# Kernel optimization log

Hardware: AMD Instinct MI355X
Metric: run time of the kernel (lower is better)

## Reference

```python
import jax, jax.numpy as jnp
import numpy as np

EMBED = 1024
HEADS = 16
HEAD_DIM = EMBED // HEADS


def setup_inputs() -> dict:
    key = jax.random.key(0)
    ks = jax.random.split(key, 6)
    s = 1.0 / np.sqrt(EMBED)
    return {
        "x": jax.random.normal(ks[0], (2, 2048, EMBED), dtype=jnp.float32),
        "Wq": jax.random.normal(ks[1], (EMBED, EMBED), dtype=jnp.float32) * s,
        "Wk": jax.random.normal(ks[2], (EMBED, EMBED), dtype=jnp.float32) * s,
        "Wv": jax.random.normal(ks[3], (EMBED, EMBED), dtype=jnp.float32) * s,
        "Wfc": jax.random.normal(ks[4], (EMBED, EMBED), dtype=jnp.float32) * s,
        "bfc": jnp.zeros((EMBED,), dtype=jnp.float32),
    }


def reference(x, Wq, Wk, Wv, Wfc, bfc):
    # x: (N, L, E). Linear(E,E,bias=False) applies y = x @ W.T (torch convention).
    N, L, E = x.shape
    q = (x @ Wq.T).reshape(N, L, HEADS, HEAD_DIM)
    k = (x @ Wk.T).reshape(N, L, HEADS, HEAD_DIM)
    v = (x @ Wv.T).reshape(N, L, HEADS, HEAD_DIM)
    # energy: (N, H, Q, K)
    energy = jnp.einsum('nqhd,nkhd->nhqk', q, k)
    # NOTE: original scales by sqrt(embed_size), not sqrt(head_dim)
    attn = jax.nn.softmax(energy / jnp.sqrt(jnp.float32(E)), axis=3)
    out = jnp.einsum('nhql,nlhd->nqhd', attn, v).reshape(N, L, E)
    return out @ Wfc.T + bfc
```

## Files before the change

kernel.cpp:

```cpp
#include <hip/hip_runtime.h>
#include <stdint.h>


typedef short bf16x8 __attribute__((ext_vector_type(8)));
typedef short bf16x4 __attribute__((ext_vector_type(4)));
typedef float f32x4 __attribute__((ext_vector_type(4)));

__device__ __forceinline__ unsigned short f2bf(float f) {
  union { float f; unsigned u; } v; v.f = f;
  return (unsigned short)((v.u + 0x7FFFu + ((v.u >> 16) & 1u)) >> 16);
}

#if defined(__has_builtin)
#if __has_builtin(__builtin_amdgcn_cvt_pk_bf16_f32)
#define HAVE_PK_BF16 1
#endif
#if __has_builtin(__builtin_amdgcn_exp2f)
#define EXP2(x) __builtin_amdgcn_exp2f(x)
#endif
#endif
#ifndef EXP2
#define EXP2(x) exp2f(x)
#endif

__device__ __forceinline__ unsigned pk2bf(float a, float b) {
#ifdef HAVE_PK_BF16
  typedef __bf16 bfv2 __attribute__((ext_vector_type(2)));
  union { bfv2 v; unsigned u; } c;
  c.v = __builtin_amdgcn_cvt_pk_bf16_f32(a, b);
  return c.u;
#else
  return (unsigned)f2bf(a) | ((unsigned)f2bf(b) << 16);
#endif
}

__device__ __forceinline__ void load_lds16(const unsigned short* g, unsigned short* l) {
  __builtin_amdgcn_global_load_lds(
      (const __attribute__((address_space(1))) unsigned int*)(const void*)g,
      (__attribute__((address_space(3))) unsigned int*)(void*)l, 16, 0, 0);
}

#define MFMA16(a, b, c) __builtin_amdgcn_mfma_f32_16x16x32_bf16((a), (b), (c), 0, 0, 0)

#if defined(__has_builtin)
#if __has_builtin(__builtin_amdgcn_mfma_f32_16x16x16bf16_1k)
#define MFMAK16(a, b, c) __builtin_amdgcn_mfma_f32_16x16x16bf16_1k((a), (b), (c), 0, 0, 0)
#elif __has_builtin(__builtin_amdgcn_mfma_f32_16x16x16_bf16)
#define MFMAK16(a, b, c) __builtin_amdgcn_mfma_f32_16x16x16_bf16((a), (b), (c), 0, 0, 0)
#endif
#endif
#ifndef MFMAK16
__device__ __forceinline__ f32x4 mfmak16_asm(bf16x4 a, bf16x4 b, f32x4 c) {
  asm volatile("v_mfma_f32_16x16x16_bf16 %0, %1, %2, %0" : "+v"(c) : "v"(a), "v"(b));
  return c;
}
#define MFMAK16(a, b, c) mfmak16_asm((a), (b), (c))
#endif

__global__ __launch_bounds__(256) void cvt_all_kernel(
    const float* __restrict__ x, const float* __restrict__ w0, const float* __restrict__ w1,
    const float* __restrict__ w2, const float* __restrict__ w3, unsigned short* __restrict__ xb,
    unsigned short* __restrict__ d0, unsigned short* __restrict__ d1,
    unsigned short* __restrict__ d2, unsigned short* __restrict__ d3) {
  int i = blockIdx.x * 256 + threadIdx.x;
  const float* s;
  unsigned short* d;
  int off;
  if (i < 1048576) {
    s = x; d = xb; off = i;
  } else {
    int j = i - 1048576;
    int w = j >> 18;
    off = j & 262143;
    s = (w == 0) ? w0 : (w == 1) ? w1 : (w == 2) ? w2 : w3;
    d = (w == 0) ? d0 : (w == 1) ? d1 : (w == 2) ? d2 : d3;
  }
  float4 f = ((const float4*)s)[off];
  uint2 o;
  o.x = pk2bf(f.x, f.y);
  o.y = pk2bf(f.z, f.w);
  ((uint2*)d)[off] = o;
}

__global__ __launch_bounds__(256) void gemm_qkv_kernel(
    const unsigned short* __restrict__ Xb, const unsigned short* __restrict__ Wqb,
    const unsigned short* __restrict__ Wkb, const unsigned short* __restrict__ Wvb,
    unsigned short* __restrict__ Qo, unsigned short* __restrict__ Ko,
    unsigned short* __restrict__ Vt) {
  __shared__ __align__(16) unsigned short As[128 * 32];
  __shared__ __align__(16) unsigned short Bs[128 * 32];
  const int mode = blockIdx.z;
  const unsigned short* W = (mode == 0) ? Wqb : ((mode == 1) ? Wkb : Wvb);
  const int n0 = blockIdx.x * 128;
  const int m0 = blockIdx.y * 128;
  const int tid = threadIdx.x;
  const int lane = tid & 63;
  const int wv = tid >> 6;
  const int wm = (wv >> 1) * 64;
  const int wn = (wv & 1) * 64;
  const int qq = lane >> 4;
  const int cc = lane & 15;

  const f32x4 fz = {0.f, 0.f, 0.f, 0.f};
  f32x4 acc[4][4];
#pragma unroll
  for (int i = 0; i < 4; i++)
#pragma unroll
    for (int j = 0; j < 4; j++) acc[i][j] = fz;

  const int ia0 = tid, ia1 = tid + 256;
  const int ra0 = ia0 >> 2, ca0 = (ia0 & 3) * 8;
  const int ra1 = ia1 >> 2, ca1 = (ia1 & 3) * 8;

  for (int k0 = 0; k0 < 1024; k0 += 32) {
    __syncthreads();
    load_lds16(Xb + (m0 + ra0) * 1024 + k0 + ca0, As + ia0 * 8);
    load_lds16(Xb + (m0 + ra1) * 1024 + k0 + ca1, As + ia1 * 8);
    load_lds16(W + (n0 + ra0) * 1024 + k0 + ca0, Bs + ia0 * 8);
    load_lds16(W + (n0 + ra1) * 1024 + k0 + ca1, Bs + ia1 * 8);
    __syncthreads();
    bf16x8 a[4], b[4];
#pragma unroll
    for (int i = 0; i < 4; i++) a[i] = *(const bf16x8*)(As + (wm + i * 16 + cc) * 32 + qq * 8);
#pragma unroll
    for (int j = 0; j < 4; j++) b[j] = *(const bf16x8*)(Bs + (wn + j * 16 + cc) * 32 + qq * 8);
    if (mode < 2) {
#pragma unroll
      for (int i = 0; i < 4; i++)
#pragma unroll
        for (int j = 0; j < 4; j++) acc[i][j] = MFMA16(b[j], a[i], acc[i][j]);
    } else {
#pragma unroll
      for (int i = 0; i < 4; i++)
#pragma unroll
        for (int j = 0; j < 4; j++) acc[i][j] = MFMA16(a[i], b[j], acc[i][j]);
    }
  }

  if (mode < 2) {
    const float esc = (mode == 0) ? 0.0450842200277801f : 1.0f;
    unsigned short* dst = (mode == 0) ? Qo : Ko;
#pragma unroll
    for (int i = 0; i < 4; i++) {
      int row = m0 + wm + i * 16 + cc;
#pragma unroll
      for (int j = 0; j < 4; j++) {
        int col = n0 + wn + j * 16 + qq * 4;
        uint2 pk;
        pk.x = pk2bf(acc[i][j][0] * esc, acc[i][j][1] * esc);
        pk.y = pk2bf(acc[i][j][2] * esc, acc[i][j][3] * esc);
        *(uint2*)(dst + row * 1024 + col) = pk;
      }
    }
  } else {
#pragma unroll
    for (int i = 0; i < 4; i++)
#pragma unroll
      for (int j = 0; j < 4; j++) {
        int row = m0 + wm + i * 16 + qq * 4;
        int nn = row >> 11, ll = row & 2047;
        int col = n0 + wn + j * 16 + cc;
        int hh = col >> 6, dd = col & 63;
        uint2 pk;
        pk.x = pk2bf(acc[i][j][0], acc[i][j][1]);
        pk.y = pk2bf(acc[i][j][2], acc[i][j][3]);
        *(uint2*)(Vt + ((nn * 16 + hh) * 64 + dd) * 2048 + ll) = pk;
      }
  }
}

__global__ __launch_bounds__(256, 2) void attn_kernel(const unsigned short* __restrict__ Qg,
                                                      const unsigned short* __restrict__ Kg,
                                                      const unsigned short* __restrict__ Vg,
                                                      unsigned short* __restrict__ Og) {
  __shared__ __align__(16) unsigned short smem[2][128 * 64 + 64 * 128];
  const int qt = blockIdx.x, hh = blockIdx.y, nb = blockIdx.z;
  const int tid = threadIdx.x, lane = tid & 63, wv = tid >> 6;
  const int pair = wv >> 1, wq = wv & 1;
  const int ptid = tid & 127;
  const int qq = lane >> 4, cc = lane & 15;
  const int q0 = qt * 128 + wq * 64;
  const int kb = pair * 1024;
  unsigned short* Kp = smem[pair];
  unsigned short* Vp = smem[pair] + 128 * 64;
  const unsigned short* Kbase = Kg + (size_t)(nb * 2048 + kb) * 1024 + hh * 64;
  const unsigned short* Vbase = Vg + (size_t)((nb * 16 + hh) * 64) * 2048 + kb;

  const int cK = ptid & 7, rKb = ptid >> 3;
  const int swK = (cK ^ (rKb & 7)) << 3;
  const int cV = ptid & 15, rVb = ptid >> 4;

  bf16x8 qf[4][2];
#pragma unroll
  for (int rt = 0; rt < 4; rt++)
#pragma unroll
    for (int kc = 0; kc < 2; kc++)
      qf[rt][kc] = *(const bf16x8*)(Qg + (size_t)(nb * 2048 + q0 + rt * 16 + cc) * 1024 +
                                    hh * 64 + kc * 32 + qq * 8);

  const f32x4 fz = {0.f, 0.f, 0.f, 0.f};
  const bf16x4 onesA = {(short)0x3F80, (short)0x3F80, (short)0x3F80, (short)0x3F80};
  f32x4 o[4][4];
  f32x4 lacc[4];
#pragma unroll
  for (int rt = 0; rt < 4; rt++) {
    lacc[rt] = fz;
#pragma unroll
    for (int vt = 0; vt < 4; vt++) o[rt][vt] = fz;
  }

  bf16x8 kbuf[8], vbuf[8];
#pragma unroll
  for (int p = 0; p < 8; p++)
    kbuf[p] = *(const bf16x8*)(Kbase + (size_t)(p * 16 + rKb) * 1024 + cK * 8);
#pragma unroll
  for (int p = 0; p < 8; p++)
    vbuf[p] = *(const bf16x8*)(Vbase + (size_t)(p * 8 + rVb) * 2048 + cV * 8);

#pragma unroll 1
  for (int it = 0; it < 8; it++) {
    __syncthreads();
#pragma unroll
    for (int p = 0; p < 8; p++) *(bf16x8*)(Kp + (p * 16 + rKb) * 64 + swK) = kbuf[p];
#pragma unroll
    for (int p = 0; p < 8; p++)
      *(bf16x8*)(Vp + (p * 8 + rVb) * 128 + ((cV ^ (((p & 1) << 3) | rVb)) << 3)) = vbuf[p];
    __syncthreads();
    if (it < 7) {
      const size_t ktn = (size_t)(it + 1) * 128;
#pragma unroll
      for (int p = 0; p < 8; p++)
        kbuf[p] = *(const bf16x8*)(Kbase + (ktn + p * 16 + rKb) * 1024 + cK * 8);
#pragma unroll
      for (int p = 0; p < 8; p++)
        vbuf[p] = *(const bf16x8*)(Vbase + (size_t)(p * 8 + rVb) * 2048 + ktn + cV * 8);
    }
#pragma unroll
    for (int st = 0; st < 8; st++) {
      const unsigned short* kr = Kp + (st * 16 + cc) * 64;
      int ch0 = (qq ^ (cc & 7)) << 3;
      bf16x8 k0 = *(const bf16x8*)(kr + ch0);
      bf16x8 k1 = *(const bf16x8*)(kr + (ch0 ^ 32));
      f32x4 z[4];
#pragma unroll
      for (int rt = 0; rt < 4; rt++) {
        z[rt] = MFMA16(k0, qf[rt][0], fz);
        z[rt] = MFMA16(k1, qf[rt][1], z[rt]);
      }
      bf16x4 bp[4];
#pragma unroll
      for (int rt = 0; rt < 4; rt++) {
        float p0 = EXP2(z[rt][0]), p1 = EXP2(z[rt][1]);
        float p2 = EXP2(z[rt][2]), p3 = EXP2(z[rt][3]);
        union { uint2 u; bf16x4 v; } pk;
        pk.u.x = pk2bf(p0, p1);
        pk.u.y = pk2bf(p2, p3);
        bp[rt] = pk.v;
        lacc[rt] = MFMAK16(onesA, bp[rt], lacc[rt]);
      }
      int vc = st * 2 + (qq >> 1);
      int voff = (qq & 1) * 4;
#pragma unroll
      for (int vt = 0; vt < 4; vt++) {
        bf16x4 vf = *(const bf16x4*)(Vp + (vt * 16 + cc) * 128 + ((vc ^ cc) << 3) + voff);
#pragma unroll
        for (int rt = 0; rt < 4; rt++) o[rt][vt] = MFMAK16(vf, bp[rt], o[rt][vt]);
      }
    }
  }

  float* oex = (float*)&smem[0][0];
  float* lex = oex + 8192;
  __syncthreads();
  if (pair == 1) {
#pragma unroll
    for (int rt = 0; rt < 4; rt++) {
#pragma unroll
      for (int vt = 0; vt < 4; vt++) {
        int idx = (((wq * 4 + rt) * 4 + vt) * 4 + qq) * 16 + cc;
        *(f32x4*)(oex + idx * 4) = o[rt][vt];
      }
      if (qq == 0) lex[(wq * 4 + rt) * 16 + cc] = lacc[rt][0];
    }
  }
  __syncthreads();
  if (pair == 0) {
#pragma unroll
    for (int rt = 0; rt < 4; rt++) {
      float rinv = 1.0f / (lacc[rt][0] + lex[(wq * 4 + rt) * 16 + cc]);
#pragma unroll
      for (int vt = 0; vt < 4; vt++) {
        int idx = (((wq * 4 + rt) * 4 + vt) * 4 + qq) * 16 + cc;
        f32x4 op = *(const f32x4*)(oex + idx * 4);
        uint2 ov;
        ov.x = pk2bf((o[rt][vt][0] + op[0]) * rinv, (o[rt][vt][1] + op[1]) * rinv);
        ov.y = pk2bf((o[rt][vt][2] + op[2]) * rinv, (o[rt][vt][3] + op[3]) * rinv);
        *(uint2*)(Og + (size_t)(nb * 2048 + q0 + rt * 16 + cc) * 1024 + hh * 64 + vt * 16 +
                  qq * 4) = ov;
      }
    }
  }
}

__global__ __launch_bounds__(256) void gemm_fc_kernel(const unsigned short* __restrict__ Ab,
                                                      const unsigned short* __restrict__ Wb,
                                                      const float* __restrict__ bias,
                                                      float* __restrict__ Co) {
  __shared__ __align__(16) unsigned short As[64 * 32];
  __shared__ __align__(16) unsigned short Bs[128 * 32];
  const int n0 = blockIdx.x * 128;
  const int m0 = blockIdx.y * 64;
  const int tid = threadIdx.x;
  const int lane = tid & 63;
  const int wv = tid >> 6;
  const int wm = (wv & 1) * 32;
  const int wn = (wv >> 1) * 64;
  const int qq = lane >> 4;
  const int cc = lane & 15;

  const f32x4 fz = {0.f, 0.f, 0.f, 0.f};
  f32x4 acc[2][4];
#pragma unroll
  for (int i = 0; i < 2; i++)
#pragma unroll
    for (int j = 0; j < 4; j++) acc[i][j] = fz;

  const int raA = tid >> 2, caA = (tid & 3) * 8;
  const int ia0 = tid, ia1 = tid + 256;
  const int rb0 = ia0 >> 2, cb0 = (ia0 & 3) * 8;
  const int rb1 = ia1 >> 2, cb1 = (ia1 & 3) * 8;

  for (int k0 = 0; k0 < 1024; k0 += 32) {
    __syncthreads();
    load_lds16(Ab + (m0 + raA) * 1024 + k0 + caA, As + tid * 8);
    load_lds16(Wb + (n0 + rb0) * 1024 + k0 + cb0, Bs + ia0 * 8);
    load_lds16(Wb + (n0 + rb1) * 1024 + k0 + cb1, Bs + ia1 * 8);
    __syncthreads();
    bf16x8 a[2], b[4];
#pragma unroll
    for (int i = 0; i < 2; i++) a[i] = *(const bf16x8*)(As + (wm + i * 16 + cc) * 32 + qq * 8);
#pragma unroll
    for (int j = 0; j < 4; j++) b[j] = *(const bf16x8*)(Bs + (wn + j * 16 + cc) * 32 + qq * 8);
#pragma unroll
    for (int i = 0; i < 2; i++)
#pragma unroll
      for (int j = 0; j < 4; j++) acc[i][j] = MFMA16(b[j], a[i], acc[i][j]);
  }

#pragma unroll
  for (int i = 0; i < 2; i++) {
    int row = m0 + wm + i * 16 + cc;
#pragma unroll
    for (int j = 0; j < 4; j++) {
      int col = n0 + wn + j * 16 + qq * 4;
      float4 bb = *(const float4*)(bias + col);
      float4 ov;
      ov.x = acc[i][j][0] + bb.x;
      ov.y = acc[i][j][1] + bb.y;
      ov.z = acc[i][j][2] + bb.z;
      ov.w = acc[i][j][3] + bb.w;
      *(float4*)(Co + (size_t)row * 1024 + col) = ov;
    }
  }
}

extern "C" void kernel_launch(void* const* d_in, const int* in_sizes, int n_in, void* d_out,
                              int out_size, void* d_ws, size_t ws_size, hipStream_t stream) {
  const float* x = (const float*)d_in[0];
  const float* Wq = (const float*)d_in[1];
  const float* Wk = (const float*)d_in[2];
  const float* Wv = (const float*)d_in[3];
  const float* Wfc = (const float*)d_in[4];
  const float* bfc = (const float*)d_in[5];
  float* out = (float*)d_out;
  char* ws = (char*)d_ws;
  unsigned short* xb = (unsigned short*)(ws);
  unsigned short* wqb = (unsigned short*)(ws + (8u << 20));
  unsigned short* wkb = (unsigned short*)(ws + (10u << 20));
  unsigned short* wvb = (unsigned short*)(ws + (12u << 20));
  unsigned short* wfb = (unsigned short*)(ws + (14u << 20));
  unsigned short* Qb = (unsigned short*)(ws + (16u << 20));
  unsigned short* Kb = (unsigned short*)(ws + (24u << 20));
  unsigned short* Vtb = (unsigned short*)(ws + (32u << 20));
  unsigned short* Ob = (unsigned short*)(ws + (40u << 20));

  cvt_all_kernel<<<8192, 256, 0, stream>>>(x, Wq, Wk, Wv, Wfc, xb, wqb, wkb, wvb, wfb);
  gemm_qkv_kernel<<<dim3(8, 32, 3), 256, 0, stream>>>(xb, wqb, wkb, wvb, Qb, Kb, Vtb);
  attn_kernel<<<dim3(16, 16, 2), 256, 0, stream>>>(Qb, Kb, Vtb, Ob);
  gemm_fc_kernel<<<dim3(8, 64), 256, 0, stream>>>(Ob, wfb, bfc, out);
}
```

Before: 212.0 us.

## Double-buffer K/V tiles via direct global-to-LDS loads and sum softmax in registers

The attention kernel now streams K and V in 64-key tiles into double-buffered shared memory using direct global-to-LDS loads, instead of staging 128-key tiles through registers. Loading the next tile while the current one is computed is meant to remove the register staging and one of the two barriers per iteration. The row-sum for the softmax denominator moves from an extra MFMA against a ones vector to scalar adds plus cross-lane shuffles at the end. This relies on a load_lds16 helper defined elsewhere, and it changes the V layout and swizzle in shared memory along with the tile size.

Result: faster. 200.8 us (-5.3%).

```diff
diff --git a/kernel.cpp b/kernel.cpp
--- a/kernel.cpp
+++ b/kernel.cpp
@@ -173,22 +173,18 @@
                                                       const unsigned short* __restrict__ Kg,
                                                       const unsigned short* __restrict__ Vg,
                                                       unsigned short* __restrict__ Og) {
-  __shared__ __align__(16) unsigned short smem[2][128 * 64 + 64 * 128];
+  __shared__ __align__(16) unsigned short smem[2][2][8192];
   const int qt = blockIdx.x, hh = blockIdx.y, nb = blockIdx.z;
   const int tid = threadIdx.x, lane = tid & 63, wv = tid >> 6;
   const int pair = wv >> 1, wq = wv & 1;
-  const int ptid = tid & 127;
   const int qq = lane >> 4, cc = lane & 15;
   const int q0 = qt * 128 + wq * 64;
-  const int kb = pair * 1024;
-  unsigned short* Kp = smem[pair];
-  unsigned short* Vp = smem[pair] + 128 * 64;
-  const unsigned short* Kbase = Kg + (size_t)(nb * 2048 + kb) * 1024 + hh * 64;
-  const unsigned short* Vbase = Vg + (size_t)((nb * 16 + hh) * 64) * 2048 + kb;
-
-  const int cK = ptid & 7, rKb = ptid >> 3;
-  const int swK = (cK ^ (rKb & 7)) << 3;
-  const int cV = ptid & 15, rVb = ptid >> 4;
+  const unsigned short* Kbase = Kg + (size_t)(nb * 2048 + pair * 1024) * 1024 + hh * 64;
+  const unsigned short* Vbase = Vg + (size_t)((nb * 16 + hh) * 64) * 2048 + pair * 1024;
+
+  const int lr = lane >> 3;
+  const int lc8 = ((lane & 7) ^ lr) * 8;
+  const int ldl = lane * 8;
 
   bf16x8 qf[4][2];
 #pragma unroll
@@ -199,44 +195,43 @@
                                     hh * 64 + kc * 32 + qq * 8);
 
   const f32x4 fz = {0.f, 0.f, 0.f, 0.f};
-  const bf16x4 onesA = {(short)0x3F80, (short)0x3F80, (short)0x3F80, (short)0x3F80};
   f32x4 o[4][4];
-  f32x4 lacc[4];
-#pragma unroll
-  for (int rt = 0; rt < 4; rt++) {
-    lacc[rt] = fz;
+  float lsum[4] = {0.f, 0.f, 0.f, 0.f};
+#pragma unroll
+  for (int rt = 0; rt < 4; rt++)
 #pragma unroll
     for (int vt = 0; vt < 4; vt++) o[rt][vt] = fz;
-  }
-
-  bf16x8 kbuf[8], vbuf[8];
-#pragma unroll
-  for (int p = 0; p < 8; p++)
-    kbuf[p] = *(const bf16x8*)(Kbase + (size_t)(p * 16 + rKb) * 1024 + cK * 8);
-#pragma unroll
-  for (int p = 0; p < 8; p++)
-    vbuf[p] = *(const bf16x8*)(Vbase + (size_t)(p * 8 + rVb) * 2048 + cV * 8);
+
+  {
+    unsigned short* Kb = &smem[pair][0][0];
+    unsigned short* Vb = &smem[pair][0][4096];
+#pragma unroll
+    for (int i = 0; i < 4; i++) {
+      int CI = wq * 4 + i;
+      load_lds16(Kbase + (size_t)(CI * 8 + lr) * 1024 + lc8, Kb + CI * 512 + ldl);
+      load_lds16(Vbase + (size_t)(CI * 8 + lr) * 2048 + lc8, Vb + CI * 512 + ldl);
+    }
+  }
+  __syncthreads();
 
 #pragma unroll 1
-  for (int it = 0; it < 8; it++) {
-    __syncthreads();
-#pragma unroll
-    for (int p = 0; p < 8; p++) *(bf16x8*)(Kp + (p * 16 + rKb) * 64 + swK) = kbuf[p];
-#pragma unroll
-    for (int p = 0; p < 8; p++)
-      *(bf16x8*)(Vp + (p * 8 + rVb) * 128 + ((cV ^ (((p & 1) << 3) | rVb)) << 3)) = vbuf[p];
-    __syncthreads();
-    if (it < 7) {
-      const size_t ktn = (size_t)(it + 1) * 128;
-#pragma unroll
-      for (int p = 0; p < 8; p++)
-        kbuf[p] = *(const bf16x8*)(Kbase + (ktn + p * 16 + rKb) * 1024 + cK * 8);
-#pragma unroll
-      for (int p = 0; p < 8; p++)
-        vbuf[p] = *(const bf16x8*)(Vbase + (size_t)(p * 8 + rVb) * 2048 + ktn + cV * 8);
-    }
-#pragma unroll
-    for (int st = 0; st < 8; st++) {
+  for (int it = 0; it < 16; it++) {
+    const int buf = it & 1;
+    if (it < 15) {
+      const int ktn = (it + 1) * 64;
+      unsigned short* Kb = &smem[pair][buf ^ 1][0];
+      unsigned short* Vb = &smem[pair][buf ^ 1][4096];
+#pragma unroll
+      for (int i = 0; i < 4; i++) {
+        int CI = wq * 4 + i;
+        load_lds16(Kbase + (size_t)(ktn + CI * 8 + lr) * 1024 + lc8, Kb + CI * 512 + ldl);
+        load_lds16(Vbase + (size_t)(CI * 8 + lr) * 2048 + ktn + lc8, Vb + CI * 512 + ldl);
+      }
+    }
+    const unsigned short* Kp = &smem[pair][buf][0];
+    const unsigned short* Vp = &smem[pair][buf][4096];
+#pragma unroll
+    for (int st = 0; st < 4; st++) {
       const unsigned short* kr = Kp + (st * 16 + cc) * 64;
       int ch0 = (qq ^ (cc & 7)) << 3;
       bf16x8 k0 = *(const bf16x8*)(kr + ch0);
@@ -252,24 +247,33 @@
       for (int rt = 0; rt < 4; rt++) {
         float p0 = EXP2(z[rt][0]), p1 = EXP2(z[rt][1]);
         float p2 = EXP2(z[rt][2]), p3 = EXP2(z[rt][3]);
+        lsum[rt] += (p0 + p1) + (p2 + p3);
         union { uint2 u; bf16x4 v; } pk;
         pk.u.x = pk2bf(p0, p1);
         pk.u.y = pk2bf(p2, p3);
         bp[rt] = pk.v;
-        lacc[rt] = MFMAK16(onesA, bp[rt], lacc[rt]);
       }
       int vc = st * 2 + (qq >> 1);
       int voff = (qq & 1) * 4;
 #pragma unroll
       for (int vt = 0; vt < 4; vt++) {
-        bf16x4 vf = *(const bf16x4*)(Vp + (vt * 16 + cc) * 128 + ((vc ^ cc) << 3) + voff);
+        bf16x4 vf = *(const bf16x4*)(Vp + (vt * 16 + cc) * 64 + ((vc ^ (cc & 7)) << 3) + voff);
 #pragma unroll
         for (int rt = 0; rt < 4; rt++) o[rt][vt] = MFMAK16(vf, bp[rt], o[rt][vt]);
       }
     }
-  }
-
-  float* oex = (float*)&smem[0][0];
+    __syncthreads();
+  }
+
+#pragma unroll
+  for (int rt = 0; rt < 4; rt++) {
+    float l = lsum[rt];
+    l += __shfl_xor(l, 16);
+    l += __shfl_xor(l, 32);
+    lsum[rt] = l;
+  }
+
+  float* oex = (float*)&smem[0][0][0];
   float* lex = oex + 8192;
   __syncthreads();
   if (pair == 1) {
@@ -280,14 +284,14 @@
         int idx = (((wq * 4 + rt) * 4 + vt) * 4 + qq) * 16 + cc;
         *(f32x4*)(oex + idx * 4) = o[rt][vt];
       }
-      if (qq == 0) lex[(wq * 4 + rt) * 16 + cc] = lacc[rt][0];
+      if (qq == 0) lex[(wq * 4 + rt) * 16 + cc] = lsum[rt];
     }
   }
   __syncthreads();
   if (pair == 0) {
 #pragma unroll
     for (int rt = 0; rt < 4; rt++) {
-      float rinv = 1.0f / (lacc[rt][0] + lex[(wq * 4 + rt) * 16 + cc]);
+      float rinv = 1.0f / (lsum[rt] + lex[(wq * 4 + rt) * 16 + cc]);
 #pragma unroll
       for (int vt = 0; vt < 4; vt++) {
         int idx = (((wq * 4 + rt) * 4 + vt) * 4 + qq) * 16 + cc;
```
